# Optimization experiments

Hardware: AMD Instinct MI355X
Metric: run time of the kernel (lower is better)

The kernel has to match this reference:

```python
import jax, jax.numpy as jnp
import numpy as np

N = 4096      # nodes
F = 64        # feature dim (= in = hidden = out channels)
DEPTH = 3
RATIO = 0.5


def _gcn(x, A, W, b):
    # GCNConv(improved=True): self-loop weight 2.0, sym-normalized propagation
    n = A.shape[0]
    A_hat = A + 2.0 * jnp.eye(n, dtype=A.dtype)
    deg = A_hat.sum(axis=1)
    dinv = jnp.where(deg > 0, jax.lax.rsqrt(deg), 0.0)
    A_norm = dinv[:, None] * A_hat * dinv[None, :]
    return A_norm @ (x @ W) + b


def _augment(A):
    # add_self_loops (fill 1.0) -> spspmm(A,A) -> remove_self_loops, dense form
    n = A.shape[0]
    eye = jnp.eye(n, dtype=A.dtype)
    A_sl = A + eye
    A2 = A_sl @ A_sl
    return A2 * (1.0 - eye)


def _topk_pool(x, A, p, ratio):
    # TopKPooling: score = tanh((x @ p)/||p||); keep top ceil(ratio*N) nodes
    score = jnp.tanh((x @ p) / jnp.linalg.norm(p))
    k = int(np.ceil(ratio * x.shape[0]))          # static
    vals, perm = jax.lax.top_k(score, k)
    x_new = x[perm] * vals[:, None]
    A_new = A[perm][:, perm]                      # filter_adj
    return x_new, A_new, perm


def setup_inputs() -> dict:
    key = jax.random.key(0)
    ks = jax.random.split(key, 9)
    x = jax.random.normal(ks[0], (N, F), dtype=jnp.float32)
    # sparse random undirected graph, avg degree ~32, no self loops
    u = jax.random.uniform(ks[1], (N, N), dtype=jnp.float32)
    m = (u < (16.0 / N)).astype(jnp.float32)
    adj = jnp.maximum(m, m.T) * (1.0 - jnp.eye(N, dtype=jnp.float32))
    s = 1.0 / np.sqrt(F)
    down_W = jax.random.normal(ks[2], (DEPTH + 1, F, F), dtype=jnp.float32) * s
    down_b = jnp.zeros((DEPTH + 1, F), dtype=jnp.float32)
    pool_w = jax.random.normal(ks[3], (DEPTH, F), dtype=jnp.float32) * s
    up_W = jax.random.normal(ks[4], (DEPTH, F, F), dtype=jnp.float32) * s
    up_b = jnp.zeros((DEPTH, F), dtype=jnp.float32)
    fc_w = jax.random.normal(ks[5], (F, 1), dtype=jnp.float32) * s
    fc_b = jnp.zeros((1,), dtype=jnp.float32)
    prob = jnp.zeros((), dtype=jnp.float32)  # dropout p = 0 -> deterministic
    return {"x": x, "adj": adj, "prob": prob, "down_W": down_W,
            "down_b": down_b, "pool_w": pool_w, "up_W": up_W,
            "up_b": up_b, "fc_w": fc_w, "fc_b": fc_b}


def reference(x, adj, prob, down_W, down_b, pool_w, up_W, up_b, fc_w, fc_b):
    act = jax.nn.relu
    A = adj
    h = act(_gcn(x, A, down_W[0], down_b[0]))
    xs, As, perms = [h], [A], []
    for i in range(DEPTH):
        A = _augment(A)
        h, A, perm = _topk_pool(h, A, pool_w[i], RATIO)
        h = act(_gcn(h, A, down_W[i + 1], down_b[i + 1]))
        if i < DEPTH - 1:
            xs.append(h); As.append(A)
        perms.append(perm)
    for i in range(DEPTH):
        j = DEPTH - 1 - i
        res, A, perm = xs[j], As[j], perms[j]
        up = jnp.zeros_like(res).at[perm].set(h)   # scatter unpool
        h = res + up                               # sum_res
        h = _gcn(h, A, up_W[i], up_b[i])
        if i < DEPTH - 1:
            h = act(h)
    h = jax.nn.relu(h)
    h = h / (1.0 - prob)   # dropout with p=prob(=0): all-ones keep mask
    return h @ fc_w + fc_b
```

## Files before the change

### kernel.cpp

```cpp
#include <hip/hip_runtime.h>
#include <cstdint>
#include <cstddef>


typedef float  f4v    __attribute__((ext_vector_type(4)));
typedef float  f32x4  __attribute__((ext_vector_type(4)));
typedef __bf16 bf16x8 __attribute__((ext_vector_type(8)));
typedef __bf16 bf16x4 __attribute__((ext_vector_type(4)));
typedef int    i32x4  __attribute__((ext_vector_type(4)));

#define NN0 4096
#define NN1 2048
#define NN2 1024
#define NN3 512

__global__ __launch_bounds__(256) void k_zs_deg(const float* __restrict__ X,
                                                const float* __restrict__ W,
                                                const float* __restrict__ A,
                                                int n,
                                                float* __restrict__ DEG,
                                                float* __restrict__ zs,
                                                __bf16* __restrict__ ADJB,
                                                __bf16* __restrict__ Zt0,
                                                __bf16* __restrict__ Zt1,
                                                __bf16* __restrict__ Zt2) {
    __shared__ float Ws[64][65];
    __shared__ float Xs[4][64];
    __shared__ float degs[4];
    int tid = threadIdx.x;
#pragma unroll
    for (int q = 0; q < 16; q++) {
        int idx = q * 256 + tid;
        Ws[idx >> 6][idx & 63] = W[idx];
    }
    int row0 = blockIdx.x << 2;
    int r = tid >> 6, lane = tid & 63;
    const float* ar = A + (size_t)(row0 + r) * n;
    __bf16* ab = ADJB + (size_t)(row0 + r) * n;
    float s = 0.f;
    for (int j = lane << 2; j < n; j += 256) {
        f4v a = *(const f4v*)(ar + j);
        s += a[0] + a[1] + a[2] + a[3];
        bf16x4 b;
#pragma unroll
        for (int e = 0; e < 4; e++) b[e] = (__bf16)a[e];
        *(bf16x4*)(ab + j) = b;
    }
#pragma unroll
    for (int off = 32; off > 0; off >>= 1) s += __shfl_xor(s, off);
    if (lane == 0) { degs[r] = s; DEG[row0 + r] = s; }
    Xs[r][lane] = X[((size_t)(row0 + r) << 6) + lane];
    __syncthreads();
    float acc = 0.f;
#pragma unroll
    for (int k = 0; k < 64; k++) acc = fmaf(Xs[r][k], Ws[k][lane], acc);
    float di = 1.0f / sqrtf(degs[r] + 2.0f);
    float zval = di * acc;
    zs[((size_t)(row0 + r) << 6) + lane] = zval;
    __syncthreads();
    Xs[r][lane] = zval;
    __syncthreads();
    int c = tid >> 2, rr = tid & 3;
    float v = Xs[rr][c];
    float v0 = (float)(__bf16)v;
    float v1 = (float)(__bf16)(v - v0);
    size_t o = (size_t)c * n + row0 + rr;
    Zt0[o] = (__bf16)v0;
    Zt1[o] = (__bf16)(v - v0);
    Zt2[o] = (__bf16)(v - v0 - v1);
}

__global__ __launch_bounds__(256) void k_zs_pool(const float* __restrict__ H,
                                                 const float* __restrict__ sc,
                                                 const int* __restrict__ perm,
                                                 const float* __restrict__ W,
                                                 const float* __restrict__ deg,
                                                 float* __restrict__ zs,
                                                 __bf16* __restrict__ Zt0,
                                                 __bf16* __restrict__ Zt1,
                                                 __bf16* __restrict__ Zt2,
                                                 int n) {
    __shared__ float Ws[64][65];
    __shared__ float Xs[4][64];
    int tid = threadIdx.x;
#pragma unroll
    for (int q = 0; q < 16; q++) {
        int idx = q * 256 + tid;
        Ws[idx >> 6][idx & 63] = W[idx];
    }
    int row0 = blockIdx.x << 2;
    int r = tid >> 6, f = tid & 63;
    int src = perm[row0 + r];
    Xs[r][f] = H[((size_t)src << 6) + f] * sc[src];
    __syncthreads();
    float acc = 0.f;
#pragma unroll
    for (int k = 0; k < 64; k++) acc = fmaf(Xs[r][k], Ws[k][f], acc);
    float di = 1.0f / sqrtf(deg[row0 + r] + 2.0f);
    float zval = di * acc;
    zs[((size_t)(row0 + r) << 6) + f] = zval;
    if (Zt0) {
        __syncthreads();
        Xs[r][f] = zval;
        __syncthreads();
        int c = tid >> 2, rr = tid & 3;
        float v = Xs[rr][c];
        float v0 = (float)(__bf16)v;
        float v1 = (float)(__bf16)(v - v0);
        size_t o = (size_t)c * n + row0 + rr;
        Zt0[o] = (__bf16)v0;
        Zt1[o] = (__bf16)(v - v0);
        Zt2[o] = (__bf16)(v - v0 - v1);
    }
}

__global__ __launch_bounds__(256) void k_zs_unpool(const float* __restrict__ RES,
                                                   const float* __restrict__ HS,
                                                   const int* __restrict__ inv,
                                                   const float* __restrict__ W,
                                                   const float* __restrict__ deg,
                                                   float* __restrict__ zs,
                                                   __bf16* __restrict__ Zt0,
                                                   __bf16* __restrict__ Zt1,
                                                   __bf16* __restrict__ Zt2,
                                                   int n) {
    __shared__ float Ws[64][65];
    __shared__ float Xs[4][64];
    int tid = threadIdx.x;
#pragma unroll
    for (int q = 0; q < 16; q++) {
        int idx = q * 256 + tid;
        Ws[idx >> 6][idx & 63] = W[idx];
    }
    int row0 = blockIdx.x << 2;
    int r = tid >> 6, f = tid & 63;
    int grow = row0 + r;
    int iv = inv[grow];
    float xv = RES[((size_t)grow << 6) + f];
    if (iv >= 0) xv += HS[((size_t)iv << 6) + f];
    Xs[r][f] = xv;
    __syncthreads();
    float acc = 0.f;
#pragma unroll
    for (int k = 0; k < 64; k++) acc = fmaf(Xs[r][k], Ws[k][f], acc);
    float di = 1.0f / sqrtf(deg[grow] + 2.0f);
    float zval = di * acc;
    zs[((size_t)grow << 6) + f] = zval;
    if (Zt0) {
        __syncthreads();
        Xs[r][f] = zval;
        __syncthreads();
        int c = tid >> 2, rr = tid & 3;
        float v = Xs[rr][c];
        float v0 = (float)(__bf16)v;
        float v1 = (float)(__bf16)(v - v0);
        size_t o = (size_t)c * n + row0 + rr;
        Zt0[o] = (__bf16)v0;
        Zt1[o] = (__bf16)(v - v0);
        Zt2[o] = (__bf16)(v - v0 - v1);
    }
}

__global__ __launch_bounds__(256) void k_prop(const float* __restrict__ A,
                                              const float* __restrict__ zs,
                                              float* __restrict__ ypart, int n) {
    int rb = blockIdx.x, ks = blockIdx.y;
    int chunk = n >> 2;
    int j0 = ks * chunk;
    __shared__ float AtT[64][68];
    __shared__ float Zt[64][68];
    int tid = threadIdx.x;
    int lr = tid >> 2;
    int lc = (tid & 3) << 4;
    int ty = tid >> 4, tx = tid & 15;
    float acc[4][4] = {};
    const float* Arow = A + (size_t)(rb * 64 + lr) * n;
    for (int jt = j0; jt < j0 + chunk; jt += 64) {
#pragma unroll
        for (int q = 0; q < 4; q++) {
            f4v av = *(const f4v*)(Arow + jt + lc + (q << 2));
#pragma unroll
            for (int e = 0; e < 4; e++) AtT[lc + (q << 2) + e][lr] = av[e];
        }
#pragma unroll
        for (int q = 0; q < 4; q++) {
            f4v zv = *(const f4v*)(zs + (((size_t)(jt + lr)) << 6) + lc + (q << 2));
            *(f4v*)&Zt[lr][lc + (q << 2)] = zv;
        }
        __syncthreads();
#pragma unroll 4
        for (int k = 0; k < 64; k++) {
            f4v a4 = *(const f4v*)&AtT[k][ty << 2];
            f4v z4 = *(const f4v*)&Zt[k][tx << 2];
#pragma unroll
            for (int r = 0; r < 4; r++)
#pragma unroll
                for (int c = 0; c < 4; c++)
                    acc[r][c] = fmaf(a4[r], z4[c], acc[r][c]);
        }
        __syncthreads();
    }
    float* yp = ypart + ((size_t)ks * n << 6);
#pragma unroll
    for (int r = 0; r < 4; r++) {
        f4v o; o[0] = acc[r][0]; o[1] = acc[r][1]; o[2] = acc[r][2]; o[3] = acc[r][3];
        *(f4v*)(yp + (((size_t)(rb * 64 + (ty << 2) + r)) << 6) + (tx << 2)) = o;
    }
}

__global__ __launch_bounds__(256) void k_propm(const __bf16* __restrict__ Ab,
                                               const __bf16* __restrict__ Zt0,
                                               const __bf16* __restrict__ Zt1,
                                               const __bf16* __restrict__ Zt2,
                                               float* __restrict__ ypart,
                                               int n, int chunk) {
    __shared__ __bf16 At[128 * 64];
    __shared__ __bf16 B0[64 * 64], B1[64 * 64], B2[64 * 64];
    int tid = threadIdx.x;
    int m0 = blockIdx.x * 128;
    int k0b = blockIdx.y * chunk;
    int wave = tid >> 6, lane = tid & 63, quad = lane >> 4, l16 = lane & 15;
    int wm = wave << 5;
    f32x4 acc[2][4] = {};
    for (int k0 = k0b; k0 < k0b + chunk; k0 += 64) {
#pragma unroll
        for (int it = 0; it < 4; it++) {
            int e = it * 256 + tid;
            int row = e >> 3, seg = e & 7;
            int sg = seg ^ (row & 7);
            const __bf16* g = Ab + ((size_t)(m0 + row) * n + k0 + (sg << 3));
            __builtin_amdgcn_global_load_lds(
                (const __attribute__((address_space(1))) void*)g,
                (__attribute__((address_space(3))) void*)(At + (e << 3)), 16, 0, 0);
        }
#pragma unroll
        for (int it = 0; it < 2; it++) {
            int e = it * 256 + tid;
            int row = e >> 3, seg = e & 7;
            int sg = seg ^ (row & 7);
            size_t off = (size_t)row * n + k0 + (sg << 3);
            __builtin_amdgcn_global_load_lds(
                (const __attribute__((address_space(1))) void*)(Zt0 + off),
                (__attribute__((address_space(3))) void*)(B0 + (e << 3)), 16, 0, 0);
            __builtin_amdgcn_global_load_lds(
                (const __attribute__((address_space(1))) void*)(Zt1 + off),
                (__attribute__((address_space(3))) void*)(B1 + (e << 3)), 16, 0, 0);
            __builtin_amdgcn_global_load_lds(
                (const __attribute__((address_space(1))) void*)(Zt2 + off),
                (__attribute__((address_space(3))) void*)(B2 + (e << 3)), 16, 0, 0);
        }
        __syncthreads();
#pragma unroll
        for (int kk = 0; kk < 2; kk++) {
            int s = (kk << 2) + quad;
            bf16x8 af[2];
#pragma unroll
            for (int im = 0; im < 2; im++) {
                int row = wm + (im << 4) + l16;
                af[im] = *(const bf16x8*)(At + (row << 6) + ((s ^ (row & 7)) << 3));
            }
#pragma unroll
            for (int cg = 0; cg < 4; cg++) {
                int brow = (cg << 4) + l16;
                int so = (s ^ (brow & 7)) << 3;
                bf16x8 b0 = *(const bf16x8*)(B0 + (brow << 6) + so);
                bf16x8 b1 = *(const bf16x8*)(B1 + (brow << 6) + so);
                bf16x8 b2 = *(const bf16x8*)(B2 + (brow << 6) + so);
#pragma unroll
                for (int im = 0; im < 2; im++) {
                    acc[im][cg] = __builtin_amdgcn_mfma_f32_16x16x32_bf16(af[im], b0, acc[im][cg], 0, 0, 0);
                    acc[im][cg] = __builtin_amdgcn_mfma_f32_16x16x32_bf16(af[im], b1, acc[im][cg], 0, 0, 0);
                    acc[im][cg] = __builtin_amdgcn_mfma_f32_16x16x32_bf16(af[im], b2, acc[im][cg], 0, 0, 0);
                }
            }
        }
        __syncthreads();
    }
    float* yp = ypart + ((size_t)blockIdx.y * n << 6);
#pragma unroll
    for (int im = 0; im < 2; im++)
#pragma unroll
        for (int cg = 0; cg < 4; cg++)
#pragma unroll
            for (int r = 0; r < 4; r++) {
                int grow = m0 + wm + (im << 4) + (quad << 2) + r;
                int gcol = (cg << 4) + l16;
                yp[((size_t)grow << 6) + gcol] = acc[im][cg][r];
            }
}

__global__ __launch_bounds__(256) void k_epi(const float* __restrict__ ypart,
                                             const float* __restrict__ zs,
                                             const float* __restrict__ deg,
                                             const float* __restrict__ b,
                                             float* __restrict__ H, int n, int S,
                                             int relu,
                                             const float* __restrict__ p,
                                             float* __restrict__ score,
                                             int* __restrict__ cnt,
                                             const float* __restrict__ fcw,
                                             const float* __restrict__ fcb,
                                             const float* __restrict__ prob,
                                             float* __restrict__ out) {
    int idx = blockIdx.x * 256 + threadIdx.x;
    int i = idx >> 6, f = idx & 63;
    size_t stride = (size_t)n << 6;
    float y = 0.f;
    for (int s2 = 0; s2 < S; s2++) y += ypart[(size_t)s2 * stride + idx];
    float di = 1.0f / sqrtf(deg[i] + 2.0f);
    float v = di * (y + 2.0f * zs[idx]) + b[f];
    if (relu) v = fmaxf(v, 0.f);
    if (H) H[idx] = v;
    if (p) {
        float pv = p[f];
        float d = v * pv, q = pv * pv;
#pragma unroll
        for (int off = 32; off > 0; off >>= 1) {
            d += __shfl_xor(d, off);
            q += __shfl_xor(q, off);
        }
        if (f == 0) score[i] = tanhf(d / sqrtf(q));
        if (idx < n) cnt[idx] = 0;
    }
    if (fcw) {
        float hv = fmaxf(v, 0.f) * fcw[f];
#pragma unroll
        for (int off = 32; off > 0; off >>= 1) hv += __shfl_xor(hv, off);
        if (f == 0) out[i] = hv / (1.0f - prob[0]) + fcb[0];
    }
}

__global__ __launch_bounds__(256) void k_gather8(const float* __restrict__ A,
                                                 const int* __restrict__ perm,
                                                 signed char* __restrict__ Mg,
                                                 int kbits4 ) {
    size_t idx16 = (size_t)blockIdx.x * 256 + threadIdx.x;
    int r = (int)(idx16 >> kbits4);
    int c = ((int)idx16 & ((1 << kbits4) - 1)) << 4;
    int K = 1 << (kbits4 + 4);
    int src = perm[r];
    const float* rowp = A + (size_t)src * K + c;
    union { signed char ch[16]; i32x4 v; } u;
#pragma unroll
    for (int q = 0; q < 4; q++) {
        f4v x = *(const f4v*)(rowp + (q << 2));
#pragma unroll
        for (int j = 0; j < 4; j++) {
            float val = x[j];
            if (src == c + (q << 2) + j) val += 1.0f;
            u.ch[(q << 2) + j] = (signed char)val;
        }
    }
    *(i32x4*)(Mg + (idx16 << 4)) = u.v;
}

__global__ __launch_bounds__(256) void k_gather(const float* __restrict__ A,
                                                const int* __restrict__ perm,
                                                __bf16* __restrict__ Mg,
                                                int kbits3 ) {
    size_t idx8 = (size_t)blockIdx.x * 256 + threadIdx.x;
    int r = (int)(idx8 >> kbits3);
    int c = ((int)idx8 & ((1 << kbits3) - 1)) << 3;
    int K = 1 << (kbits3 + 3);
    int src = perm[r];
    const float* rowp = A + (size_t)src * K + c;
    f4v v0 = *(const f4v*)rowp;
    f4v v1 = *(const f4v*)(rowp + 4);
    bf16x8 t;
#pragma unroll
    for (int j = 0; j < 4; j++) {
        float v = v0[j]; if (src == c + j) v += 1.0f; t[j] = (__bf16)v;
    }
#pragma unroll
    for (int j = 0; j < 4; j++) {
        float v = v1[j]; if (src == c + 4 + j) v += 1.0f; t[4 + j] = (__bf16)v;
    }
    *(bf16x8*)(Mg + idx8 * 8) = t;
}

template<int BN>
__global__ __launch_bounds__(256) void k_augmm_i8(const signed char* __restrict__ Mg,
                                                  float* __restrict__ C,
                                                  __bf16* __restrict__ Cb,
                                                  float* __restrict__ DEG,
                                                  int nk, int K) {
    __shared__ signed char At[64 * 64];
    __shared__ signed char Bt[BN * 64];
    constexpr int NI = BN / 32;
    int tid = threadIdx.x;
    int m0 = blockIdx.x * 64, n0 = blockIdx.y * BN;
    int wave = tid >> 6, lane = tid & 63;
    int wm = (wave >> 1) << 5;
    int wn = (wave & 1) * (BN >> 1);
    int quad = lane >> 4, l16 = lane & 15;
    i32x4 acc[2][NI] = {};
    for (int k0 = 0; k0 < K; k0 += 64) {
        {
            int e = tid;
            int row = e >> 2, cs = e & 3;
            int cg = cs ^ ((row & 3) ^ ((row >> 2) & 3));
            const signed char* g = Mg + ((size_t)(m0 + row) * K + k0 + (cg << 4));
            __builtin_amdgcn_global_load_lds(
                (const __attribute__((address_space(1))) void*)g,
                (__attribute__((address_space(3))) void*)(At + (e << 4)), 16, 0, 0);
        }
#pragma unroll
        for (int it = 0; it < BN / 64; it++) {
            int e = it * 256 + tid;
            int row = e >> 2, cs = e & 3;
            int cg = cs ^ ((row & 3) ^ ((row >> 2) & 3));
            const signed char* g = Mg + ((size_t)(n0 + row) * K + k0 + (cg << 4));
            __builtin_amdgcn_global_load_lds(
                (const __attribute__((address_space(1))) void*)g,
                (__attribute__((address_space(3))) void*)(Bt + (e << 4)), 16, 0, 0);
        }
        __syncthreads();
        i32x4 af[2], bf[NI];
#pragma unroll
        for (int im = 0; im < 2; im++) {
            int row = wm + (im << 4) + l16;
            int sl = quad ^ ((row & 3) ^ ((row >> 2) & 3));
            af[im] = *(const i32x4*)(At + (row << 6) + (sl << 4));
        }
#pragma unroll
        for (int in2 = 0; in2 < NI; in2++) {
            int row = wn + (in2 << 4) + l16;
            int sl = quad ^ ((row & 3) ^ ((row >> 2) & 3));
            bf[in2] = *(const i32x4*)(Bt + (row << 6) + (sl << 4));
        }
#pragma unroll
        for (int im = 0; im < 2; im++)
#pragma unroll
            for (int in2 = 0; in2 < NI; in2++)
                acc[im][in2] = __builtin_amdgcn_mfma_i32_16x16x64_i8(
                    af[im], bf[in2], acc[im][in2], 0, 0, 0);
        __syncthreads();
    }
#pragma unroll
    for (int im = 0; im < 2; im++) {
#pragma unroll
        for (int r = 0; r < 4; r++) {
            int grow = m0 + wm + (im << 4) + (quad << 2) + r;
            int part = 0;
#pragma unroll
            for (int in2 = 0; in2 < NI; in2++) {
                int gcol = n0 + wn + (in2 << 4) + l16;
                int v = (grow == gcol) ? 0 : acc[im][in2][r];
                C[(size_t)grow * nk + gcol] = (float)v;
                if (Cb) Cb[(size_t)grow * nk + gcol] = (__bf16)(float)v;
                part += v;
            }
#pragma unroll
            for (int off = 8; off > 0; off >>= 1) part += __shfl_xor(part, off);
            if (l16 == 0) atomicAdd(&DEG[grow], (float)part);
        }
    }
}

__global__ __launch_bounds__(256) void k_augmm_bf(const __bf16* __restrict__ Mg,
                                                  float* __restrict__ C,
                                                  float* __restrict__ DEG,
                                                  int nk, int K) {
    constexpr int BN = 64;
    __shared__ __bf16 At[64 * 64];
    __shared__ __bf16 Bt[BN * 64];
    constexpr int NI = BN / 32;
    int tid = threadIdx.x;
    int m0 = blockIdx.x * 64, n0 = blockIdx.y * BN;
    int wave = tid >> 6, lane = tid & 63;
    int wm = (wave >> 1) << 5;
    int wn = (wave & 1) * (BN >> 1);
    int quad = lane >> 4, l16 = lane & 15;
    f32x4 acc[2][NI] = {};
    for (int k0 = 0; k0 < K; k0 += 64) {
#pragma unroll
        for (int it = 0; it < 2; it++) {
            int e = it * 256 + tid;
            int row = e >> 3, seg = e & 7;
            int sg = seg ^ (row & 7);
            const __bf16* g = Mg + ((size_t)(m0 + row) * K + k0 + (sg << 3));
            __builtin_amdgcn_global_load_lds(
                (const __attribute__((address_space(1))) void*)g,
                (__attribute__((address_space(3))) void*)(At + (e << 3)), 16, 0, 0);
        }
#pragma unroll
        for (int it = 0; it < BN / 32; it++) {
            int e = it * 256 + tid;
            int row = e >> 3, seg = e & 7;
            int sg = seg ^ (row & 7);
            const __bf16* g = Mg + ((size_t)(n0 + row) * K + k0 + (sg << 3));
            __builtin_amdgcn_global_load_lds(
                (const __attribute__((address_space(1))) void*)g,
                (__attribute__((address_space(3))) void*)(Bt + (e << 3)), 16, 0, 0);
        }
        __syncthreads();
#pragma unroll
        for (int kk = 0; kk < 2; kk++) {
            int s = (kk << 2) + quad;
            bf16x8 af[2], bfm[NI];
#pragma unroll
            for (int im = 0; im < 2; im++) {
                int row = wm + (im << 4) + l16;
                af[im] = *(const bf16x8*)(At + (row << 6) + ((s ^ (row & 7)) << 3));
            }
#pragma unroll
            for (int in2 = 0; in2 < NI; in2++) {
                int row = wn + (in2 << 4) + l16;
                bfm[in2] = *(const bf16x8*)(Bt + (row << 6) + ((s ^ (row & 7)) << 3));
            }
#pragma unroll
            for (int im = 0; im < 2; im++)
#pragma unroll
                for (int in2 = 0; in2 < NI; in2++)
                    acc[im][in2] = __builtin_amdgcn_mfma_f32_16x16x32_bf16(
                        af[im], bfm[in2], acc[im][in2], 0, 0, 0);
        }
        __syncthreads();
    }
#pragma unroll
    for (int im = 0; im < 2; im++) {
#pragma unroll
        for (int r = 0; r < 4; r++) {
            int grow = m0 + wm + (im << 4) + (quad << 2) + r;
            float part = 0.f;
#pragma unroll
            for (int in2 = 0; in2 < NI; in2++) {
                int gcol = n0 + wn + (in2 << 4) + l16;
                float v = (grow == gcol) ? 0.f : acc[im][in2][r];
                C[(size_t)grow * nk + gcol] = v;
                part += v;
            }
#pragma unroll
            for (int off = 8; off > 0; off >>= 1) part += __shfl_xor(part, off);
            if (l16 == 0) atomicAdd(&DEG[grow], part);
        }
    }
}

__global__ __launch_bounds__(256) void k_topk_count(const float* __restrict__ score,
                                                    int* __restrict__ cnt, int n) {
    __shared__ float sc[256];
    int j0 = blockIdx.y * 256;
    sc[threadIdx.x] = score[j0 + threadIdx.x];
    int i = blockIdx.x * 256 + threadIdx.x;
    float si = score[i];
    __syncthreads();
    int c = 0;
#pragma unroll 8
    for (int t = 0; t < 256; t++) {
        float sj = sc[t];
        int j = j0 + t;
        c += ((sj > si) || (sj == si && j < i)) ? 1 : 0;
    }
    atomicAdd(&cnt[i], c);
}
__global__ __launch_bounds__(256) void k_topk_scatter(const int* __restrict__ cnt,
                                                      int* __restrict__ perm,
                                                      int* __restrict__ inv,
                                                      float* __restrict__ degN,
                                                      int k) {
    int i = blockIdx.x * 256 + threadIdx.x;
    int c = cnt[i];
    if (c < k) perm[c] = i;
    inv[i] = (c < k) ? c : -1;
    if (i < k) degN[i] = 0.f;
}

extern "C" void kernel_launch(void* const* d_in, const int* in_sizes, int n_in,
                              void* d_out, int out_size, void* d_ws, size_t ws_size,
                              hipStream_t stream) {
    (void)in_sizes; (void)n_in; (void)out_size;
    const float* x     = (const float*)d_in[0];
    const float* adj   = (const float*)d_in[1];
    const float* prob  = (const float*)d_in[2];
    const float* downW = (const float*)d_in[3];
    const float* downb = (const float*)d_in[4];
    const float* poolw = (const float*)d_in[5];
    const float* upW   = (const float*)d_in[6];
    const float* upb   = (const float*)d_in[7];
    const float* fcw   = (const float*)d_in[8];
    const float* fcb   = (const float*)d_in[9];

    char* ws = (char*)d_ws;
    signed char* MG8 = (signed char*)(ws + 0);
    __bf16* MGB  = (__bf16*)(ws + 0);
    float*  A1   = (float*)(ws + 8388608);
    float*  A2   = (float*)(ws + 25165824);
    float*  A3   = (float*)(ws + 29360128);
    __bf16* ADJB = (__bf16*)(ws + 30408704);
    __bf16* A1B  = (__bf16*)(ws + 63963136);
    float*  H0   = (float*)(ws + 72351744);
    float*  H1   = (float*)(ws + 73400320);
    float*  H2   = (float*)(ws + 73924608);
    float*  H3   = (float*)(ws + 74186752);
    float*  ZS   = (float*)(ws + 74317824);
    __bf16* ZT0  = (__bf16*)(ws + 75366400);
    __bf16* ZT1  = (__bf16*)(ws + 75890688);
    __bf16* ZT2  = (__bf16*)(ws + 76414976);
    float*  YP   = (float*)(ws + 76939264);
    float*  UA   = (float*)(ws + 93716480);
    float*  UB   = (float*)(ws + 94240768);
    float*  DEG0 = (float*)(ws + 94765056);
    float*  DEG1 = (float*)(ws + 94781440);
    float*  DEG2 = (float*)(ws + 94789632);
    float*  DEG3 = (float*)(ws + 94793728);
    float*  SCORE= (float*)(ws + 94795776);
    int*    PERM0= (int*)(ws + 94812160);
    int*    PERM1= (int*)(ws + 94820352);
    int*    PERM2= (int*)(ws + 94824448);
    int*    INV0 = (int*)(ws + 94826496);
    int*    INV1 = (int*)(ws + 94842880);
    int*    INV2 = (int*)(ws + 94851072);
    int*    CNT  = (int*)(ws + 94855168);
    if (ws_size < (size_t)94871552) return;

    k_zs_deg<<<NN0 / 4, 256, 0, stream>>>(x, downW, adj, NN0, DEG0, ZS,
                                          ADJB, ZT0, ZT1, ZT2);
    k_propm<<<dim3(NN0 / 128, 16), 256, 0, stream>>>(ADJB, ZT0, ZT1, ZT2, YP, NN0, 256);
    k_epi<<<NN0 / 4, 256, 0, stream>>>(YP, ZS, DEG0, downb, H0, NN0, 16, 1,
                                       poolw + 0, SCORE, CNT,
                                       nullptr, nullptr, nullptr, nullptr);
    k_topk_count<<<dim3(NN0 / 256, NN0 / 256), 256, 0, stream>>>(SCORE, CNT, NN0);
    k_topk_scatter<<<NN0 / 256, 256, 0, stream>>>(CNT, PERM0, INV0, DEG1, NN1);
    k_gather8<<<(NN1 * NN0 / 16) / 256, 256, 0, stream>>>(adj, PERM0, MG8, 8);
    k_augmm_i8<128><<<dim3(NN1 / 64, NN1 / 128), 256, 0, stream>>>(MG8, A1, A1B, DEG1, NN1, NN0);
    k_zs_pool<<<NN1 / 4, 256, 0, stream>>>(H0, SCORE, PERM0, downW + 4096, DEG1, ZS,
                                           ZT0, ZT1, ZT2, NN1);
    k_propm<<<dim3(NN1 / 128, 32), 256, 0, stream>>>(A1B, ZT0, ZT1, ZT2, YP, NN1, 64);
    k_epi<<<NN1 / 4, 256, 0, stream>>>(YP, ZS, DEG1, downb + 64, H1, NN1, 32, 1,
                                       poolw + 64, SCORE, CNT,
                                       nullptr, nullptr, nullptr, nullptr);
    k_topk_count<<<dim3(NN1 / 256, NN1 / 256), 256, 0, stream>>>(SCORE, CNT, NN1);
    k_topk_scatter<<<NN1 / 256, 256, 0, stream>>>(CNT, PERM1, INV1, DEG2, NN2);
    k_gather8<<<(NN2 * NN1 / 16) / 256, 256, 0, stream>>>(A1, PERM1, MG8, 7);
    k_augmm_i8<64><<<dim3(NN2 / 64, NN2 / 64), 256, 0, stream>>>(MG8, A2, nullptr, DEG2, NN2, NN1);
    k_zs_pool<<<NN2 / 4, 256, 0, stream>>>(H1, SCORE, PERM1, downW + 2 * 4096, DEG2, ZS,
                                           nullptr, nullptr, nullptr, NN2);
    k_prop<<<dim3(NN2 / 64, 4), 256, 0, stream>>>(A2, ZS, YP, NN2);
    k_epi<<<NN2 / 4, 256, 0, stream>>>(YP, ZS, DEG2, downb + 2 * 64, H2, NN2, 4, 1,
                                       poolw + 128, SCORE, CNT,
                                       nullptr, nullptr, nullptr, nullptr);
    k_topk_count<<<dim3(NN2 / 256, NN2 / 256), 256, 0, stream>>>(SCORE, CNT, NN2);
    k_topk_scatter<<<NN2 / 256, 256, 0, stream>>>(CNT, PERM2, INV2, DEG3, NN3);
    k_gather<<<(NN3 * NN2 / 8) / 256, 256, 0, stream>>>(A2, PERM2, MGB, 7);
    k_augmm_bf<<<dim3(NN3 / 64, NN3 / 64), 256, 0, stream>>>(MGB, A3, DEG3, NN3, NN2);
    k_zs_pool<<<NN3 / 4, 256, 0, stream>>>(H2, SCORE, PERM2, downW + 3 * 4096, DEG3, ZS,
                                           nullptr, nullptr, nullptr, NN3);
    k_prop<<<dim3(NN3 / 64, 4), 256, 0, stream>>>(A3, ZS, YP, NN3);
    k_epi<<<NN3 / 4, 256, 0, stream>>>(YP, ZS, DEG3, downb + 3 * 64, H3, NN3, 4, 1,
                                       nullptr, nullptr, nullptr,
                                       nullptr, nullptr, nullptr, nullptr);

    k_zs_unpool<<<NN2 / 4, 256, 0, stream>>>(H2, H3, INV2, upW, DEG2, ZS,
                                             nullptr, nullptr, nullptr, NN2);
    k_prop<<<dim3(NN2 / 64, 4), 256, 0, stream>>>(A2, ZS, YP, NN2);
    k_epi<<<NN2 / 4, 256, 0, stream>>>(YP, ZS, DEG2, upb, UA, NN2, 4, 1,
                                       nullptr, nullptr, nullptr,
                                       nullptr, nullptr, nullptr, nullptr);
    k_zs_unpool<<<NN1 / 4, 256, 0, stream>>>(H1, UA, INV1, upW + 4096, DEG1, ZS,
                                             ZT0, ZT1, ZT2, NN1);
    k_propm<<<dim3(NN1 / 128, 32), 256, 0, stream>>>(A1B, ZT0, ZT1, ZT2, YP, NN1, 64);
    k_epi<<<NN1 / 4, 256, 0, stream>>>(YP, ZS, DEG1, upb + 64, UB, NN1, 32, 1,
                                       nullptr, nullptr, nullptr,
                                       nullptr, nullptr, nullptr, nullptr);
    k_zs_unpool<<<NN0 / 4, 256, 0, stream>>>(H0, UB, INV0, upW + 2 * 4096, DEG0, ZS,
                                             ZT0, ZT1, ZT2, NN0);
    k_propm<<<dim3(NN0 / 128, 16), 256, 0, stream>>>(ADJB, ZT0, ZT1, ZT2, YP, NN0, 256);
    k_epi<<<NN0 / 4, 256, 0, stream>>>(YP, ZS, DEG0, upb + 2 * 64, nullptr, NN0, 16, 0,
                                       nullptr, nullptr, nullptr,
                                       fcw, fcb, prob, (float*)d_out);
}
```

Baseline: 382.2 us.

## Fuse top-k kernels, drop fp32 A1, widen int8 K-tile, use 2-way bf16 split upsweep

Merges the top-k count and scatter kernels into one, with a last-block ticket counter doing the scatter. Stops writing the fp32 A1 matrix and gathers level-2 input from the bf16 copy instead. Widens the int8 augment GEMM K-tile from 64 to 128 to halve the barrier count. Uses a 2-term bf16 split instead of 3 for the up-path propagations, which reduces MFMA work and Z traffic but lowers precision in those layers.

```diff
diff --git a/kernel.cpp b/kernel.cpp
--- a/kernel.cpp
+++ b/kernel.cpp
@@ -110,7 +110,7 @@
         size_t o = (size_t)c * n + row0 + rr;
         Zt0[o] = (__bf16)v0;
         Zt1[o] = (__bf16)(v - v0);
-        Zt2[o] = (__bf16)(v - v0 - v1);
+        if (Zt2) Zt2[o] = (__bf16)(v - v0 - v1);
     }
 }
 
@@ -157,7 +157,7 @@
         size_t o = (size_t)c * n + row0 + rr;
         Zt0[o] = (__bf16)v0;
         Zt1[o] = (__bf16)(v - v0);
-        Zt2[o] = (__bf16)(v - v0 - v1);
+        if (Zt2) Zt2[o] = (__bf16)(v - v0 - v1);
     }
 }
 
@@ -208,14 +208,16 @@
     }
 }
 
-__global__ __launch_bounds__(256) void k_propm(const __bf16* __restrict__ Ab,
-                                               const __bf16* __restrict__ Zt0,
+template<int NP>
+__global__ __launch_bounds__(256) void k_propm(const __bf16* __restrict__ Zt0,
                                                const __bf16* __restrict__ Zt1,
                                                const __bf16* __restrict__ Zt2,
+                                               const __bf16* __restrict__ Ab,
                                                float* __restrict__ ypart,
                                                int n, int chunk) {
     __shared__ __bf16 At[128 * 64];
-    __shared__ __bf16 B0[64 * 64], B1[64 * 64], B2[64 * 64];
+    __shared__ __bf16 B[NP][64 * 64];
+    const __bf16* Zp[3] = {Zt0, Zt1, Zt2};
     int tid = threadIdx.x;
     int m0 = blockIdx.x * 128;
     int k0b = blockIdx.y * chunk;
@@ -239,15 +241,11 @@
             int row = e >> 3, seg = e & 7;
             int sg = seg ^ (row & 7);
             size_t off = (size_t)row * n + k0 + (sg << 3);
-            __builtin_amdgcn_global_load_lds(
-                (const __attribute__((address_space(1))) void*)(Zt0 + off),
-                (__attribute__((address_space(3))) void*)(B0 + (e << 3)), 16, 0, 0);
-            __builtin_amdgcn_global_load_lds(
-                (const __attribute__((address_space(1))) void*)(Zt1 + off),
-                (__attribute__((address_space(3))) void*)(B1 + (e << 3)), 16, 0, 0);
-            __builtin_amdgcn_global_load_lds(
-                (const __attribute__((address_space(1))) void*)(Zt2 + off),
-                (__attribute__((address_space(3))) void*)(B2 + (e << 3)), 16, 0, 0);
+#pragma unroll
+            for (int p = 0; p < NP; p++)
+                __builtin_amdgcn_global_load_lds(
+                    (const __attribute__((address_space(1))) void*)(Zp[p] + off),
+                    (__attribute__((address_space(3))) void*)(B[p] + (e << 3)), 16, 0, 0);
         }
         __syncthreads();
 #pragma unroll
@@ -263,14 +261,13 @@
             for (int cg = 0; cg < 4; cg++) {
                 int brow = (cg << 4) + l16;
                 int so = (s ^ (brow & 7)) << 3;
-                bf16x8 b0 = *(const bf16x8*)(B0 + (brow << 6) + so);
-                bf16x8 b1 = *(const bf16x8*)(B1 + (brow << 6) + so);
-                bf16x8 b2 = *(const bf16x8*)(B2 + (brow << 6) + so);
-#pragma unroll
-                for (int im = 0; im < 2; im++) {
-                    acc[im][cg] = __builtin_amdgcn_mfma_f32_16x16x32_bf16(af[im], b0, acc[im][cg], 0, 0, 0);
-                    acc[im][cg] = __builtin_amdgcn_mfma_f32_16x16x32_bf16(af[im], b1, acc[im][cg], 0, 0, 0);
-                    acc[im][cg] = __builtin_amdgcn_mfma_f32_16x16x32_bf16(af[im], b2, acc[im][cg], 0, 0, 0);
+#pragma unroll
+                for (int p = 0; p < NP; p++) {
+                    bf16x8 bv = *(const bf16x8*)(B[p] + (brow << 6) + so);
+#pragma unroll
+                    for (int im = 0; im < 2; im++)
+                        acc[im][cg] = __builtin_amdgcn_mfma_f32_16x16x32_bf16(
+                            af[im], bv, acc[im][cg], 0, 0, 0);
                 }
             }
         }
@@ -298,6 +295,7 @@
                                              const float* __restrict__ p,
                                              float* __restrict__ score,
                                              int* __restrict__ cnt,
+                                             int* __restrict__ tick,
                                              const float* __restrict__ fcw,
                                              const float* __restrict__ fcb,
                                              const float* __restrict__ prob,
@@ -321,12 +319,53 @@
         }
         if (f == 0) score[i] = tanhf(d / sqrtf(q));
         if (idx < n) cnt[idx] = 0;
+        if (idx == 0) *tick = 0;
     }
     if (fcw) {
         float hv = fmaxf(v, 0.f) * fcw[f];
 #pragma unroll
         for (int off = 32; off > 0; off >>= 1) hv += __shfl_xor(hv, off);
         if (f == 0) out[i] = hv / (1.0f - prob[0]) + fcb[0];
+    }
+}
+
+__global__ __launch_bounds__(256) void k_topk(const float* __restrict__ score,
+                                              int* __restrict__ cnt,
+                                              int* __restrict__ perm,
+                                              int* __restrict__ inv,
+                                              float* __restrict__ degN,
+                                              int* __restrict__ tick,
+                                              int n, int k) {
+    __shared__ float sc[256];
+    __shared__ int lastFlag;
+    int j0 = blockIdx.y * 256;
+    sc[threadIdx.x] = score[j0 + threadIdx.x];
+    int i = blockIdx.x * 256 + threadIdx.x;
+    float si = score[i];
+    __syncthreads();
+    int c = 0;
+#pragma unroll 8
+    for (int t = 0; t < 256; t++) {
+        float sj = sc[t];
+        int j = j0 + t;
+        c += ((sj > si) || (sj == si && j < i)) ? 1 : 0;
+    }
+    atomicAdd(&cnt[i], c);
+    __threadfence();
+    if (threadIdx.x == 0) {
+        int t = atomicAdd(tick, 1);
+        lastFlag = (t == (int)(gridDim.x * gridDim.y) - 1);
+    }
+    __syncthreads();
+    if (lastFlag) {
+        __threadfence();
+        for (int i2 = threadIdx.x; i2 < n; i2 += 256) {
+            int cv = __hip_atomic_load(&cnt[i2], __ATOMIC_ACQUIRE,
+                                       __HIP_MEMORY_SCOPE_AGENT);
+            if (cv < k) perm[cv] = i2;
+            inv[i2] = (cv < k) ? cv : -1;
+            if (i2 < k) degN[i2] = 0.f;
+        }
     }
 }
 
@@ -350,6 +389,34 @@
             if (src == c + (q << 2) + j) val += 1.0f;
             u.ch[(q << 2) + j] = (signed char)val;
         }
+    }
+    *(i32x4*)(Mg + (idx16 << 4)) = u.v;
+}
+
+__global__ __launch_bounds__(256) void k_gather8b(const __bf16* __restrict__ Ab,
+                                                  const int* __restrict__ perm,
+                                                  signed char* __restrict__ Mg,
+                                                  int kbits4 ) {
+    size_t idx16 = (size_t)blockIdx.x * 256 + threadIdx.x;
+    int r = (int)(idx16 >> kbits4);
+    int c = ((int)idx16 & ((1 << kbits4) - 1)) << 4;
+    int K = 1 << (kbits4 + 4);
+    int src = perm[r];
+    const __bf16* rowp = Ab + (size_t)src * K + c;
+    bf16x8 a0 = *(const bf16x8*)rowp;
+    bf16x8 a1 = *(const bf16x8*)(rowp + 8);
+    union { signed char ch[16]; i32x4 v; } u;
+#pragma unroll
+    for (int j = 0; j < 8; j++) {
+        float val = (float)a0[j];
+        if (src == c + j) val += 1.0f;
+        u.ch[j] = (signed char)val;
+    }
+#pragma unroll
+    for (int j = 0; j < 8; j++) {
+        float val = (float)a1[j];
+        if (src == c + 8 + j) val += 1.0f;
+        u.ch[8 + j] = (signed char)val;
     }
     *(i32x4*)(Mg + (idx16 << 4)) = u.v;
 }
@@ -384,8 +451,8 @@
                                                   __bf16* __restrict__ Cb,
                                                   float* __restrict__ DEG,
                                                   int nk, int K) {
-    __shared__ signed char At[64 * 64];
-    __shared__ signed char Bt[BN * 64];
+    __shared__ signed char At[64 * 128];
+    __shared__ signed char Bt[BN * 128];
     constexpr int NI = BN / 32;
     int tid = threadIdx.x;
     int m0 = blockIdx.x * 64, n0 = blockIdx.y * BN;
@@ -394,46 +461,49 @@
     int wn = (wave & 1) * (BN >> 1);
     int quad = lane >> 4, l16 = lane & 15;
     i32x4 acc[2][NI] = {};
-    for (int k0 = 0; k0 < K; k0 += 64) {
-        {
-            int e = tid;
-            int row = e >> 2, cs = e & 3;
-            int cg = cs ^ ((row & 3) ^ ((row >> 2) & 3));
+    for (int k0 = 0; k0 < K; k0 += 128) {
+#pragma unroll
+        for (int it = 0; it < 2; it++) {
+            int e = it * 256 + tid;
+            int row = e >> 3, cs = e & 7;
+            int cg = cs ^ (row & 7);
             const signed char* g = Mg + ((size_t)(m0 + row) * K + k0 + (cg << 4));
             __builtin_amdgcn_global_load_lds(
                 (const __attribute__((address_space(1))) void*)g,
                 (__attribute__((address_space(3))) void*)(At + (e << 4)), 16, 0, 0);
         }
 #pragma unroll
-        for (int it = 0; it < BN / 64; it++) {
+        for (int it = 0; it < BN / 32; it++) {
             int e = it * 256 + tid;
-            int row = e >> 2, cs = e & 3;
-            int cg = cs ^ ((row & 3) ^ ((row >> 2) & 3));
+            int row = e >> 3, cs = e & 7;
+            int cg = cs ^ (row & 7);
             const signed char* g = Mg + ((size_t)(n0 + row) * K + k0 + (cg << 4));
             __builtin_amdgcn_global_load_lds(
                 (const __attribute__((address_space(1))) void*)g,
                 (__attribute__((address_space(3))) void*)(Bt + (e << 4)), 16, 0, 0);
         }
         __syncthreads();
-        i32x4 af[2], bf[NI];
-#pragma unroll
-        for (int im = 0; im < 2; im++) {
-            int row = wm + (im << 4) + l16;
-            int sl = quad ^ ((row & 3) ^ ((row >> 2) & 3));
-            af[im] = *(const i32x4*)(At + (row << 6) + (sl << 4));
-        }
-#pragma unroll
-        for (int in2 = 0; in2 < NI; in2++) {
-            int row = wn + (in2 << 4) + l16;
-            int sl = quad ^ ((row & 3) ^ ((row >> 2) & 3));
-            bf[in2] = *(const i32x4*)(Bt + (row << 6) + (sl << 4));
-        }
-#pragma unroll
-        for (int im = 0; im < 2; im++)
-#pragma unroll
-            for (int in2 = 0; in2 < NI; in2++)
-                acc[im][in2] = __builtin_amdgcn_mfma_i32_16x16x64_i8(
-                    af[im], bf[in2], acc[im][in2], 0, 0, 0);
+#pragma unroll
+        for (int h = 0; h < 2; h++) {
+            int cix = (h << 2) + quad;
+            i32x4 af[2], bf[NI];
+#pragma unroll
+            for (int im = 0; im < 2; im++) {
+                int row = wm + (im << 4) + l16;
+                af[im] = *(const i32x4*)(At + (row << 7) + ((cix ^ (row & 7)) << 4));
+            }
+#pragma unroll
+            for (int in2 = 0; in2 < NI; in2++) {
+                int row = wn + (in2 << 4) + l16;
+                bf[in2] = *(const i32x4*)(Bt + (row << 7) + ((cix ^ (row & 7)) << 4));
+            }
+#pragma unroll
+            for (int im = 0; im < 2; im++)
+#pragma unroll
+                for (int in2 = 0; in2 < NI; in2++)
+                    acc[im][in2] = __builtin_amdgcn_mfma_i32_16x16x64_i8(
+                        af[im], bf[in2], acc[im][in2], 0, 0, 0);
+        }
         __syncthreads();
     }
 #pragma unroll
@@ -446,7 +516,7 @@
             for (int in2 = 0; in2 < NI; in2++) {
                 int gcol = n0 + wn + (in2 << 4) + l16;
                 int v = (grow == gcol) ? 0 : acc[im][in2][r];
-                C[(size_t)grow * nk + gcol] = (float)v;
+                if (C)  C[(size_t)grow * nk + gcol] = (float)v;
                 if (Cb) Cb[(size_t)grow * nk + gcol] = (__bf16)(float)v;
                 part += v;
             }
@@ -537,35 +607,6 @@
     }
 }
 
-__global__ __launch_bounds__(256) void k_topk_count(const float* __restrict__ score,
-                                                    int* __restrict__ cnt, int n) {
-    __shared__ float sc[256];
-    int j0 = blockIdx.y * 256;
-    sc[threadIdx.x] = score[j0 + threadIdx.x];
-    int i = blockIdx.x * 256 + threadIdx.x;
-    float si = score[i];
-    __syncthreads();
-    int c = 0;
-#pragma unroll 8
-    for (int t = 0; t < 256; t++) {
-        float sj = sc[t];
-        int j = j0 + t;
-        c += ((sj > si) || (sj == si && j < i)) ? 1 : 0;
-    }
-    atomicAdd(&cnt[i], c);
-}
-__global__ __launch_bounds__(256) void k_topk_scatter(const int* __restrict__ cnt,
-                                                      int* __restrict__ perm,
-                                                      int* __restrict__ inv,
-                                                      float* __restrict__ degN,
-                                                      int k) {
-    int i = blockIdx.x * 256 + threadIdx.x;
-    int c = cnt[i];
-    if (c < k) perm[c] = i;
-    inv[i] = (c < k) ? c : -1;
-    if (i < k) degN[i] = 0.f;
-}
-
 extern "C" void kernel_launch(void* const* d_in, const int* in_sizes, int n_in,
                               void* d_out, int out_size, void* d_ws, size_t ws_size,
                               hipStream_t stream) {
@@ -584,7 +625,6 @@
     char* ws = (char*)d_ws;
     signed char* MG8 = (signed char*)(ws + 0);
     __bf16* MGB  = (__bf16*)(ws + 0);
-    float*  A1   = (float*)(ws + 8388608);
     float*  A2   = (float*)(ws + 25165824);
     float*  A3   = (float*)(ws + 29360128);
     __bf16* ADJB = (__bf16*)(ws + 30408704);
@@ -612,61 +652,59 @@
     int*    INV1 = (int*)(ws + 94842880);
     int*    INV2 = (int*)(ws + 94851072);
     int*    CNT  = (int*)(ws + 94855168);
-    if (ws_size < (size_t)94871552) return;
+    int*    TICK = (int*)(ws + 94871552);
+    if (ws_size < (size_t)94871808) return;
 
     k_zs_deg<<<NN0 / 4, 256, 0, stream>>>(x, downW, adj, NN0, DEG0, ZS,
                                           ADJB, ZT0, ZT1, ZT2);
-    k_propm<<<dim3(NN0 / 128, 16), 256, 0, stream>>>(ADJB, ZT0, ZT1, ZT2, YP, NN0, 256);
+    k_propm<3><<<dim3(NN0 / 128, 16), 256, 0, stream>>>(ZT0, ZT1, ZT2, ADJB, YP, NN0, 256);
     k_epi<<<NN0 / 4, 256, 0, stream>>>(YP, ZS, DEG0, downb, H0, NN0, 16, 1,
-                                       poolw + 0, SCORE, CNT,
+                                       poolw + 0, SCORE, CNT, TICK,
                                        nullptr, nullptr, nullptr, nullptr);
-    k_topk_count<<<dim3(NN0 / 256, NN0 / 256), 256, 0, stream>>>(SCORE, CNT, NN0);
-    k_topk_scatter<<<NN0 / 256, 256, 0, stream>>>(CNT, PERM0, INV0, DEG1, NN1);
+    k_topk<<<dim3(NN0 / 256, NN0 / 256), 256, 0, stream>>>(SCORE, CNT, PERM0, INV0, DEG1, TICK, NN0, NN1);
     k_gather8<<<(NN1 * NN0 / 16) / 256, 256, 0, stream>>>(adj, PERM0, MG8, 8);
-    k_augmm_i8<128><<<dim3(NN1 / 64, NN1 / 128), 256, 0, stream>>>(MG8, A1, A1B, DEG1, NN1, NN0);
+    k_augmm_i8<128><<<dim3(NN1 / 64, NN1 / 128), 256, 0, stream>>>(MG8, nullptr, A1B, DEG1, NN1, NN0);
     k_zs_pool<<<NN1 / 4, 256, 0, stream>>>(H0, SCORE, PERM0, downW + 4096, DEG1, ZS,
                                            ZT0, ZT1, ZT2, NN1);
-    k_propm<<<dim3(NN1 / 128, 32), 256, 0, stream>>>(A1B, ZT0, ZT1, ZT2, YP, NN1, 64);
+    k_propm<3><<<dim3(NN1 / 128, 32), 256, 0, stream>>>(ZT0, ZT1, ZT2, A1B, YP, NN1, 64);
     k_epi<<<NN1 / 4, 256, 0, stream>>>(YP, ZS, DEG1, downb + 64, H1, NN1, 32, 1,
-                                       poolw + 64, SCORE, CNT,
+                                       poolw + 64, SCORE, CNT, TICK,
                                        nullptr, nullptr, nullptr, nullptr);
-    k_topk_count<<<dim3(NN1 / 256, NN1 / 256), 256, 0, stream>>>(SCORE, CNT, NN1);
-    k_topk_scatter<<<NN1 / 256, 256, 0, stream>>>(CNT, PERM1, INV1, DEG2, NN2);
-    k_gather8<<<(NN2 * NN1 / 16) / 256, 256, 0, stream>>>(A1, PERM1, MG8, 7);
+    k_topk<<<dim3(NN1 / 256, NN1 / 256), 256, 0, stream>>>(SCORE, CNT, PERM1, INV1, DEG2, TICK, NN1, NN2);
+    k_gather8b<<<(NN2 * NN1 / 16) / 256, 256, 0, stream>>>(A1B, PERM1, MG8, 7);
     k_augmm_i8<64><<<dim3(NN2 / 64, NN2 / 64), 256, 0, stream>>>(MG8, A2, nullptr, DEG2, NN2, NN1);
     k_zs_pool<<<NN2 / 4, 256, 0, stream>>>(H1, SCORE, PERM1, downW + 2 * 4096, DEG2, ZS,
                                            nullptr, nullptr, nullptr, NN2);
     k_prop<<<dim3(NN2 / 64, 4), 256, 0, stream>>>(A2, ZS, YP, NN2);
     k_epi<<<NN2 / 4, 256, 0, stream>>>(YP, ZS, DEG2, downb + 2 * 64, H2, NN2, 4, 1,
-                                       poolw + 128, SCORE, CNT,
+                                       poolw + 128, SCORE, CNT, TICK,
                                        nullptr, nullptr, nullptr, nullptr);
-    k_topk_count<<<dim3(NN2 / 256, NN2 / 256), 256, 0, stream>>>(SCORE, CNT, NN2);
-    k_topk_scatter<<<NN2 / 256, 256, 0, stream>>>(CNT, PERM2, INV2, DEG3, NN3);
+    k_topk<<<dim3(NN2 / 256, NN2 / 256), 256, 0, stream>>>(SCORE, CNT, PERM2, INV2, DEG3, TICK, NN2, NN3);
     k_gather<<<(NN3 * NN2 / 8) / 256, 256, 0, stream>>>(A2, PERM2, MGB, 7);
     k_augmm_bf<<<dim3(NN3 / 64, NN3 / 64), 256, 0, stream>>>(MGB, A3, DEG3, NN3, NN2);
     k_zs_pool<<<NN3 / 4, 256, 0, stream>>>(H2, SCORE, PERM2, downW + 3 * 4096, DEG3, ZS,
                                            nullptr, nullptr, nullptr, NN3);
     k_prop<<<dim3(NN3 / 64, 4), 256, 0, stream>>>(A3, ZS, YP, NN3);
     k_epi<<<NN3 / 4, 256, 0, stream>>>(YP, ZS, DEG3, downb + 3 * 64, H3, NN3, 4, 1,
-                                       nullptr, nullptr, nullptr,
+                                       nullptr, nullptr, nullptr, nullptr,
                                        nullptr, nullptr, nullptr, nullptr);
 
     k_zs_unpool<<<NN2 / 4, 256, 0, stream>>>(H2, H3, INV2, upW, DEG2, ZS,
                                              nullptr, nullptr, nullptr, NN2);
     k_prop<<<dim3(NN2 / 64, 4), 256, 0, stream>>>(A2, ZS, YP, NN2);
     k_epi<<<NN2 / 4, 256, 0, stream>>>(YP, ZS, DEG2, upb, UA, NN2, 4, 1,
-                                       nullptr, nullptr, nullptr,
+                                       nullptr, nullptr, nullptr, nullptr,
                                        nullptr, nullptr, nullptr, nullptr);
     k_zs_unpool<<<NN1 / 4, 256, 0, stream>>>(H1, UA, INV1, upW + 4096, DEG1, ZS,
-                                             ZT0, ZT1, ZT2, NN1);
-    k_propm<<<dim3(NN1 / 128, 32), 256, 0, stream>>>(A1B, ZT0, ZT1, ZT2, YP, NN1, 64);
+                                             ZT0, ZT1, nullptr, NN1);
+    k_propm<2><<<dim3(NN1 / 128, 32), 256, 0, stream>>>(ZT0, ZT1, nullptr, A1B, YP, NN1, 64);
     k_epi<<<NN1 / 4, 256, 0, stream>>>(YP, ZS, DEG1, upb + 64, UB, NN1, 32, 1,
-                                       nullptr, nullptr, nullptr,
+                                       nullptr, nullptr, nullptr, nullptr,
                                        nullptr, nullptr, nullptr, nullptr);
     k_zs_unpool<<<NN0 / 4, 256, 0, stream>>>(H0, UB, INV0, upW + 2 * 4096, DEG0, ZS,
-                                             ZT0, ZT1, ZT2, NN0);
-    k_propm<<<dim3(NN0 / 128, 16), 256, 0, stream>>>(ADJB, ZT0, ZT1, ZT2, YP, NN0, 256);
+                                             ZT0, ZT1, nullptr, NN0);
+    k_propm<2><<<dim3(NN0 / 128, 16), 256, 0, stream>>>(ZT0, ZT1, nullptr, ADJB, YP, NN0, 256);
     k_epi<<<NN0 / 4, 256, 0, stream>>>(YP, ZS, DEG0, upb + 2 * 64, nullptr, NN0, 16, 0,
-                                       nullptr, nullptr, nullptr,
+                                       nullptr, nullptr, nullptr, nullptr,
                                        fcw, fcb, prob, (float*)d_out);
 }
```

Measured after the change: 402.7 us. 5.4% more time.
